# Kernel tuning notes

Hardware: AMD Instinct MI355X
Metric: run time of the kernel (lower is better)

## Reference

```python
import jax, jax.numpy as jnp
import numpy as np

N, D, K = 65536, 512, 512


def _l2norm(x, eps=1e-12):
    # matches torch F.normalize: x / max(||x||, eps)
    n = jnp.linalg.norm(x, axis=-1, keepdims=True)
    return x / jnp.maximum(n, eps)


def setup_inputs() -> dict:
    key = jax.random.key(0)
    k1, k2 = jax.random.split(key)
    return {
        "embeddings": jax.random.normal(k1, (N, D), dtype=jnp.float32),
        "labels": jax.random.randint(k2, (N,), 0, K),
        "w": jnp.asarray(10.0, dtype=jnp.float32),
        "b": jnp.asarray(-5.0, dtype=jnp.float32),
        "num_classes": K,
    }


def reference(embeddings, labels, w, b, num_classes):
    # assumes labels take all values in [0, num_classes) so torch.unique's
    # inverse == labels (holds for the generated inputs: 65536 draws over 512 ids)
    labels = labels.astype(jnp.int32)
    n = embeddings.shape[0]
    emb = _l2norm(embeddings)                                        # [N, D]
    ones = jnp.ones((n,), dtype=emb.dtype)
    counts = jax.ops.segment_sum(ones, labels, num_segments=num_classes)   # [K]
    sums = jax.ops.segment_sum(emb, labels, num_segments=num_classes)      # [K, D]
    centroids = sums / jnp.maximum(counts, 1.0)[:, None]             # [K, D] (NOT re-normalized, per source)
    sims = emb @ centroids.T                                          # [N, K]
    # exclusive centroid for each sample's own class, vectorized over N
    cnt_i = counts[labels]                                            # [N]
    denom = jnp.maximum(cnt_i - 1.0, 1.0)[:, None]
    excl = _l2norm((sums[labels] - emb) / denom)                      # [N, D]
    own = jnp.sum(emb * excl, axis=-1)                                # [N]
    rows = jnp.arange(n)
    cur = sims[rows, labels]
    own = jnp.where(cnt_i > 1.0, own, cur)                            # skip singleton classes
    sims = sims.at[rows, labels].set(own)
    logits = jnp.maximum(w, 1e-6) * sims + b
    logp = jax.nn.log_softmax(logits, axis=-1)
    return -jnp.mean(logp[rows, labels])
```

## Files before the change

### kernel.cpp

```cpp
#include <hip/hip_runtime.h>
#include <hip/hip_bf16.h>

#define N_ROWS 65536
#define DIM    512
#define KCLS   512
#define BUCKET 256
#define CLOG   6.0f

typedef __bf16 bf16x8 __attribute__((ext_vector_type(8)));
typedef float  f32x16 __attribute__((ext_vector_type(16)));

__device__ __forceinline__ float bf2f(ushort u) {
    union { unsigned int i; float f; } v; v.i = ((unsigned int)u) << 16; return v.f;
}

__global__ __launch_bounds__(256) void rnorm_embb_kernel(
    const float* __restrict__ emb, const int* __restrict__ labels,
    ushort* __restrict__ embb, int* __restrict__ counts,
    ushort* __restrict__ order16)
{
    const int tid  = threadIdx.x;
    const int wave = tid >> 6;
    const int lane = tid & 63;
    const int row  = blockIdx.x * 4 + wave;

    const float4* ep = (const float4*)(emb + (size_t)row * DIM + lane * 8);
    const float4 e0 = ep[0], e1 = ep[1];
    float ss = e0.x*e0.x + e0.y*e0.y + e0.z*e0.z + e0.w*e0.w
             + e1.x*e1.x + e1.y*e1.y + e1.z*e1.z + e1.w*e1.w;
    #pragma unroll
    for (int off = 1; off < 64; off <<= 1)
        ss += __shfl_xor(ss, off, 64);
    const float rn = 1.0f / fmaxf(sqrtf(ss), 1e-12f);

    bf16x8 h;
    h[0] = (__bf16)(e0.x * rn); h[1] = (__bf16)(e0.y * rn);
    h[2] = (__bf16)(e0.z * rn); h[3] = (__bf16)(e0.w * rn);
    h[4] = (__bf16)(e1.x * rn); h[5] = (__bf16)(e1.y * rn);
    h[6] = (__bf16)(e1.z * rn); h[7] = (__bf16)(e1.w * rn);
    *(bf16x8*)(embb + (size_t)row * DIM + lane * 8) = h;

    if (lane == 0) {
        const int l   = labels[row];
        const int pos = atomicAdd(&counts[l], 1);
        order16[l * BUCKET + pos] = (ushort)row;
    }
}

__global__ __launch_bounds__(256) void class_sum_kernel(
    const ushort* __restrict__ embb,
    const int* __restrict__ counts, const ushort* __restrict__ order16,
    float* __restrict__ sums, ushort* __restrict__ centb,
    float* __restrict__ S2c)
{
    __shared__ float part[4][DIM];
    __shared__ float s2p[4];

    const int cls  = blockIdx.x;
    const int tid  = threadIdx.x;
    const int wave = tid >> 6;
    const int lane = tid & 63;
    const int cnt  = counts[cls];
    const int base = cls * BUCKET;
    const int d8   = lane * 8;

    float a0v[8] = {}, a1v[8] = {}, a2v[8] = {}, a3v[8] = {};
    int j = wave;
    for (; j + 12 < cnt; j += 16) {
        const int r1 = order16[base + j];
        const int r2 = order16[base + j + 4];
        const int r3 = order16[base + j + 8];
        const int r4 = order16[base + j + 12];
        const uint4 u1 = *(const uint4*)(embb + (size_t)r1 * DIM + d8);
        const uint4 u2 = *(const uint4*)(embb + (size_t)r2 * DIM + d8);
        const uint4 u3 = *(const uint4*)(embb + (size_t)r3 * DIM + d8);
        const uint4 u4 = *(const uint4*)(embb + (size_t)r4 * DIM + d8);
        const ushort* s1 = (const ushort*)&u1;
        const ushort* s2 = (const ushort*)&u2;
        const ushort* s3 = (const ushort*)&u3;
        const ushort* s4 = (const ushort*)&u4;
        #pragma unroll
        for (int q = 0; q < 8; ++q) {
            a0v[q] += bf2f(s1[q]); a1v[q] += bf2f(s2[q]);
            a2v[q] += bf2f(s3[q]); a3v[q] += bf2f(s4[q]);
        }
    }
    for (; j < cnt; j += 4) {
        const int r = order16[base + j];
        const uint4 u = *(const uint4*)(embb + (size_t)r * DIM + d8);
        const ushort* s1 = (const ushort*)&u;
        #pragma unroll
        for (int q = 0; q < 8; ++q) a0v[q] += bf2f(s1[q]);
    }
    #pragma unroll
    for (int q = 0; q < 8; ++q)
        part[wave][d8 + q] = (a0v[q] + a1v[q]) + (a2v[q] + a3v[q]);
    __syncthreads();

    const int d0 = tid * 2;
    const float s0 = part[0][d0]   + part[1][d0]   + part[2][d0]   + part[3][d0];
    const float s1 = part[0][d0+1] + part[1][d0+1] + part[2][d0+1] + part[3][d0+1];
    *(float2*)(sums + (size_t)cls * DIM + d0) = make_float2(s0, s1);
    const float cinv = 1.0f / fmaxf((float)cnt, 1.0f);
    const __bf16 c0 = (__bf16)(s0 * cinv);
    const __bf16 c1 = (__bf16)(s1 * cinv);
    ushort2 cpk;
    cpk.x = *(const ushort*)&c0;
    cpk.y = *(const ushort*)&c1;
    *(ushort2*)(centb + (size_t)cls * DIM + d0) = cpk;

    float p = s0 * s0 + s1 * s1;
    #pragma unroll
    for (int off = 1; off < 64; off <<= 1)
        p += __shfl_xor(p, off, 64);
    if ((tid & 63) == 0) s2p[wave] = p;
    __syncthreads();
    if (tid == 0) S2c[cls] = s2p[0] + s2p[1] + s2p[2] + s2p[3];
}

#define BM   128
#define BN   128
#define BK   64

#define GLDS(g_, l_)                                                          \
    __builtin_amdgcn_global_load_lds(                                         \
        (const __attribute__((address_space(1))) unsigned int*)(g_),          \
        (__attribute__((address_space(3))) unsigned int*)(l_), 16, 0, 0)

#define MFMA(d_, a_, b_) d_ = __builtin_amdgcn_mfma_f32_32x32x16_bf16(a_, b_, d_, 0, 0, 0)

__global__ __launch_bounds__(256, 3) void fused_loss_kernel(
    const ushort* __restrict__ embb, const int* __restrict__ labels,
    const ushort* __restrict__ centb,
    const float* __restrict__ wp, const float* __restrict__ bp,
    float* __restrict__ srow4, float* __restrict__ llgemm)
{
    __shared__ __align__(16) ushort A_lds[8192];
    __shared__ __align__(16) ushort B_lds[8192];
    __shared__ float s_ws[2][BM];
    __shared__ int   lbl_s[BM];

    const int tid  = threadIdx.x;
    const int wid  = tid >> 6;
    const int ln31 = tid & 31;
    const int half = (tid & 63) >> 5;

    const int xcd   = blockIdx.x & 7;
    const int seq   = blockIdx.x >> 3;
    const int panel = seq & 3;
    const int rb    = (seq >> 2) * 8 + xcd;
    const int r0    = rb * BM;
    const int c0    = panel * BN;

    const float wv = fmaxf(wp[0], 1e-6f);
    const float bv = bp[0];

    const ushort* aS[4];
    const ushort* bS[4];
    #pragma unroll
    for (int s = 0; s < 4; ++s) {
        const int G = tid + 256 * s;
        const int R = G >> 4;
        const int q = (G & 15) ^ (R & 15);
        const int r = ((q >> 3) << 6) | R;
        const int j = q & 7;
        aS[s] = embb  + (size_t)(r0 + r) * DIM + j * 8;
        bS[s] = centb + (size_t)(c0 + r) * DIM + j * 8;
    }

    #define STAGE(T_)                                                         \
        { _Pragma("unroll") for (int s = 0; s < 4; ++s) {                     \
            GLDS(aS[s] + (T_) * BK, &A_lds[wid * 512 + s * 2048]);            \
            GLDS(bS[s] + (T_) * BK, &B_lds[wid * 512 + s * 2048]); } }

    const int rg = wid >> 1, cg = wid & 1;
    const int rOff0 = ln31 * 256;
    const int rOff1 = (32 + ln31) * 256;
    const int px    = ln31 & 15;

    f32x16 acc[2][2] = {};

    #pragma unroll 1
    for (int t = 0; t < 8; ++t) {
        STAGE(t);
        __syncthreads();
        const char* aR = (const char*)&A_lds[0];
        const char* bR = (const char*)&B_lds[0];
        #pragma unroll
        for (int ks = 0; ks < 4; ++ks) {
            const int j  = ks * 2 + half;
            const int oA = ((rg * 8 + j) ^ px) << 4;
            const int oB = ((cg * 8 + j) ^ px) << 4;
            const bf16x8 a0 = *(const bf16x8*)(aR + rOff0 + oA);
            const bf16x8 a1 = *(const bf16x8*)(aR + rOff1 + oA);
            const bf16x8 b0 = *(const bf16x8*)(bR + rOff0 + oB);
            const bf16x8 b1 = *(const bf16x8*)(bR + rOff1 + oB);
            MFMA(acc[0][0], a0, b0); MFMA(acc[0][1], a0, b1);
            MFMA(acc[1][0], a1, b0); MFMA(acc[1][1], a1, b1);
        }
        __syncthreads();
    }

    if (tid < BM) lbl_s[tid] = labels[r0 + tid];
    __syncthreads();

    #pragma unroll
    for (int mt = 0; mt < 2; ++mt) {
        #pragma unroll
        for (int reg = 0; reg < 16; ++reg) {
            const int rowc = rg * 64 + mt * 32 + (reg & 3) + 8 * (reg >> 2) + 4 * half;
            const int lloc = lbl_s[rowc] - c0;
            const float v0 = wv * acc[mt][0][reg] + bv;
            const float v1 = wv * acc[mt][1][reg] + bv;
            const int cc = cg * 64 + ln31;
            if (cc == lloc)      llgemm[r0 + rowc] = v0;
            if (cc + 32 == lloc) llgemm[r0 + rowc] = v1;
            float e = __expf(v0 - CLOG) + __expf(v1 - CLOG);
            #pragma unroll
            for (int off = 1; off < 32; off <<= 1)
                e += __shfl_xor(e, off, 64);
            if (ln31 == 0) s_ws[cg][rowc] = e;
        }
    }
    __syncthreads();
    if (tid < BM)
        srow4[(size_t)panel * N_ROWS + r0 + tid] = s_ws[0][tid] + s_ws[1][tid];
}

__global__ __launch_bounds__(256) void merge_loss_kernel(
    const int* __restrict__ labels, const int* __restrict__ counts,
    const float* __restrict__ S2c, const float* __restrict__ srow4,
    const float* __restrict__ llgemm,
    const float* __restrict__ wp, const float* __restrict__ bp,
    float* __restrict__ partial)
{
    __shared__ float red[4];
    const int tid = threadIdx.x;
    const int row = blockIdx.x * 256 + tid;

    const float wv = fmaxf(wp[0], 1e-6f);
    const float bv = bp[0];

    const int lbl = labels[row];
    const int cnt = counts[lbl];
    const float lg = llgemm[row];
    float s = srow4[row] + srow4[N_ROWS + row]
            + srow4[2 * N_ROWS + row] + srow4[3 * N_ROWS + row];
    float ll = lg;
    if (cnt > 1) {
        const float dot = (lg - bv) / wv;
        const float q   = (float)cnt * dot;
        const float nrm = sqrtf(fmaxf(S2c[lbl] - 2.0f * q + 1.0f, 0.0f));
        const float own = (q - 1.0f) / fmaxf(nrm, 1e-12f);
        const float vown = wv * own + bv;
        s += __expf(vown - CLOG) - __expf(lg - CLOG);
        ll = vown;
    }
    float lsum = __logf(s) + CLOG - ll;
    #pragma unroll
    for (int off = 32; off > 0; off >>= 1)
        lsum += __shfl_down(lsum, off, 64);
    if ((tid & 63) == 0) red[tid >> 6] = lsum;
    __syncthreads();
    if (tid == 0)
        partial[blockIdx.x] = red[0] + red[1] + red[2] + red[3];
}

__global__ __launch_bounds__(256) void final_loss_kernel(
    const float* __restrict__ partial, float* __restrict__ out)
{
    __shared__ float red[4];
    const int tid = threadIdx.x;
    float a = partial[tid];
    #pragma unroll
    for (int off = 32; off > 0; off >>= 1)
        a += __shfl_down(a, off, 64);
    if ((tid & 63) == 0) red[tid >> 6] = a;
    __syncthreads();
    if (tid == 0)
        out[0] = (red[0] + red[1] + red[2] + red[3]) / (float)N_ROWS;
}

extern "C" void kernel_launch(void* const* d_in, const int* in_sizes, int n_in,
                              void* d_out, int out_size, void* d_ws, size_t ws_size,
                              hipStream_t stream)
{
    const float* emb    = (const float*)d_in[0];
    const int*   labels = (const int*)d_in[1];
    const float* wp     = (const float*)d_in[2];
    const float* bp     = (const float*)d_in[3];
    float* out = (float*)d_out;

    char* ws = (char*)d_ws;
    ushort* embb    = (ushort*)(ws + 0);
    ushort* order16 = (ushort*)(ws + 67108864);
    float*  sums    = (float*) (ws + 67371008);
    ushort* centb   = (ushort*)(ws + 68419584);
    int*    counts  = (int*)   (ws + 68943872);
    float*  partial = (float*) (ws + 68950016);
    float*  llgemm  = (float*) (ws + 69212160);
    float*  srow4   = (float*) (ws + 69474304);
    float*  S2c     = (float*) (ws + 70522880);

    hipMemsetAsync(counts, 0, 2048, stream);

    rnorm_embb_kernel<<<N_ROWS / 4, 256, 0, stream>>>(emb, labels, embb, counts, order16);
    class_sum_kernel<<<KCLS, 256, 0, stream>>>(embb, counts, order16, sums, centb, S2c);
    fused_loss_kernel<<<2048, 256, 0, stream>>>(embb, labels, centb, wp, bp, srow4, llgemm);
    merge_loss_kernel<<<N_ROWS / 256, 256, 0, stream>>>(labels, counts, S2c, srow4,
                                                        llgemm, wp, bp, partial);
    final_loss_kernel<<<1, 256, 0, stream>>>(partial, out);
}
```

Before: 275.6 us.

## Widen class-sum blocks, drop unused sums, fold final reduction into merge

The class-sum kernel now runs 16 waves per class instead of 4. Each wave takes 4 consecutive rows per step, and the kernel no longer writes the float sums array, which nothing else reads. The separate final-reduction kernel is removed: each merge block bumps an atomic counter, and the last block to finish reduces the per-block partials and writes the loss. This saves one kernel launch and one unused global write, at the cost of a threadfence/atomic per block and an extra zeroed counter in the workspace.

```diff
diff --git a/kernel.cpp b/kernel.cpp
--- a/kernel.cpp
+++ b/kernel.cpp
@@ -47,14 +47,13 @@
     }
 }
 
-__global__ __launch_bounds__(256) void class_sum_kernel(
+__global__ __launch_bounds__(1024) void class_sum_kernel(
     const ushort* __restrict__ embb,
     const int* __restrict__ counts, const ushort* __restrict__ order16,
-    float* __restrict__ sums, ushort* __restrict__ centb,
-    float* __restrict__ S2c)
-{
-    __shared__ float part[4][DIM];
-    __shared__ float s2p[4];
+    ushort* __restrict__ centb, float* __restrict__ S2c)
+{
+    __shared__ float part[16][DIM];
+    __shared__ float s2p[8];
 
     const int cls  = blockIdx.x;
     const int tid  = threadIdx.x;
@@ -65,12 +64,12 @@
     const int d8   = lane * 8;
 
     float a0v[8] = {}, a1v[8] = {}, a2v[8] = {}, a3v[8] = {};
-    int j = wave;
-    for (; j + 12 < cnt; j += 16) {
+    int j = wave * 4;
+    for (; j + 3 < cnt; j += 64) {
         const int r1 = order16[base + j];
-        const int r2 = order16[base + j + 4];
-        const int r3 = order16[base + j + 8];
-        const int r4 = order16[base + j + 12];
+        const int r2 = order16[base + j + 1];
+        const int r3 = order16[base + j + 2];
+        const int r4 = order16[base + j + 3];
         const uint4 u1 = *(const uint4*)(embb + (size_t)r1 * DIM + d8);
         const uint4 u2 = *(const uint4*)(embb + (size_t)r2 * DIM + d8);
         const uint4 u3 = *(const uint4*)(embb + (size_t)r3 * DIM + d8);
@@ -85,8 +84,8 @@
             a2v[q] += bf2f(s3[q]); a3v[q] += bf2f(s4[q]);
         }
     }
-    for (; j < cnt; j += 4) {
-        const int r = order16[base + j];
+    for (int t2 = j; t2 < cnt; ++t2) {
+        const int r = order16[base + t2];
         const uint4 u = *(const uint4*)(embb + (size_t)r * DIM + d8);
         const ushort* s1 = (const ushort*)&u;
         #pragma unroll
@@ -97,25 +96,26 @@
         part[wave][d8 + q] = (a0v[q] + a1v[q]) + (a2v[q] + a3v[q]);
     __syncthreads();
 
-    const int d0 = tid * 2;
-    const float s0 = part[0][d0]   + part[1][d0]   + part[2][d0]   + part[3][d0];
-    const float s1 = part[0][d0+1] + part[1][d0+1] + part[2][d0+1] + part[3][d0+1];
-    *(float2*)(sums + (size_t)cls * DIM + d0) = make_float2(s0, s1);
-    const float cinv = 1.0f / fmaxf((float)cnt, 1.0f);
-    const __bf16 c0 = (__bf16)(s0 * cinv);
-    const __bf16 c1 = (__bf16)(s1 * cinv);
-    ushort2 cpk;
-    cpk.x = *(const ushort*)&c0;
-    cpk.y = *(const ushort*)&c1;
-    *(ushort2*)(centb + (size_t)cls * DIM + d0) = cpk;
-
-    float p = s0 * s0 + s1 * s1;
-    #pragma unroll
-    for (int off = 1; off < 64; off <<= 1)
-        p += __shfl_xor(p, off, 64);
-    if ((tid & 63) == 0) s2p[wave] = p;
-    __syncthreads();
-    if (tid == 0) S2c[cls] = s2p[0] + s2p[1] + s2p[2] + s2p[3];
+    if (tid < DIM) {
+        float s = 0.f;
+        #pragma unroll
+        for (int w = 0; w < 16; ++w) s += part[w][tid];
+        const float cinv = 1.0f / fmaxf((float)cnt, 1.0f);
+        const __bf16 c = (__bf16)(s * cinv);
+        centb[(size_t)cls * DIM + tid] = *(const ushort*)&c;
+        float p = s * s;
+        #pragma unroll
+        for (int off = 1; off < 64; off <<= 1)
+            p += __shfl_xor(p, off, 64);
+        if (lane == 0) s2p[wave] = p;
+    }
+    __syncthreads();
+    if (tid == 0) {
+        float t = 0.f;
+        #pragma unroll
+        for (int w = 0; w < 8; ++w) t += s2p[w];
+        S2c[cls] = t;
+    }
 }
 
 #define BM   128
@@ -232,9 +232,11 @@
     const float* __restrict__ S2c, const float* __restrict__ srow4,
     const float* __restrict__ llgemm,
     const float* __restrict__ wp, const float* __restrict__ bp,
-    float* __restrict__ partial)
+    float* __restrict__ partial, int* __restrict__ done,
+    float* __restrict__ out)
 {
     __shared__ float red[4];
+    __shared__ int   last_s;
     const int tid = threadIdx.x;
     const int row = blockIdx.x * 256 + tid;
 
@@ -262,23 +264,23 @@
         lsum += __shfl_down(lsum, off, 64);
     if ((tid & 63) == 0) red[tid >> 6] = lsum;
     __syncthreads();
-    if (tid == 0)
+    if (tid == 0) {
         partial[blockIdx.x] = red[0] + red[1] + red[2] + red[3];
-}
-
-__global__ __launch_bounds__(256) void final_loss_kernel(
-    const float* __restrict__ partial, float* __restrict__ out)
-{
-    __shared__ float red[4];
-    const int tid = threadIdx.x;
-    float a = partial[tid];
-    #pragma unroll
-    for (int off = 32; off > 0; off >>= 1)
-        a += __shfl_down(a, off, 64);
-    if ((tid & 63) == 0) red[tid >> 6] = a;
-    __syncthreads();
-    if (tid == 0)
-        out[0] = (red[0] + red[1] + red[2] + red[3]) / (float)N_ROWS;
+        __threadfence();
+        last_s = (atomicAdd(done, 1) == (N_ROWS / 256) - 1) ? 1 : 0;
+    }
+    __syncthreads();
+    if (last_s) {
+        float a = __hip_atomic_load(&partial[tid], __ATOMIC_RELAXED,
+                                    __HIP_MEMORY_SCOPE_AGENT);
+        #pragma unroll
+        for (int off = 32; off > 0; off >>= 1)
+            a += __shfl_down(a, off, 64);
+        if ((tid & 63) == 0) red[tid >> 6] = a;
+        __syncthreads();
+        if (tid == 0)
+            out[0] = (red[0] + red[1] + red[2] + red[3]) / (float)N_ROWS;
+    }
 }
 
 extern "C" void kernel_launch(void* const* d_in, const int* in_sizes, int n_in,
@@ -294,20 +296,20 @@
     char* ws = (char*)d_ws;
     ushort* embb    = (ushort*)(ws + 0);
     ushort* order16 = (ushort*)(ws + 67108864);
-    float*  sums    = (float*) (ws + 67371008);
     ushort* centb   = (ushort*)(ws + 68419584);
     int*    counts  = (int*)   (ws + 68943872);
+    int*    done    = (int*)   (ws + 68945924);
     float*  partial = (float*) (ws + 68950016);
     float*  llgemm  = (float*) (ws + 69212160);
     float*  srow4   = (float*) (ws + 69474304);
     float*  S2c     = (float*) (ws + 70522880);
 
-    hipMemsetAsync(counts, 0, 2048, stream);
+    hipMemsetAsync(counts, 0, 2056, stream);
 
     rnorm_embb_kernel<<<N_ROWS / 4, 256, 0, stream>>>(emb, labels, embb, counts, order16);
-    class_sum_kernel<<<KCLS, 256, 0, stream>>>(embb, counts, order16, sums, centb, S2c);
+    class_sum_kernel<<<KCLS, 1024, 0, stream>>>(embb, counts, order16, centb, S2c);
     fused_loss_kernel<<<2048, 256, 0, stream>>>(embb, labels, centb, wp, bp, srow4, llgemm);
     merge_loss_kernel<<<N_ROWS / 256, 256, 0, stream>>>(labels, counts, S2c, srow4,
-                                                        llgemm, wp, bp, partial);
-    final_loss_kernel<<<1, 256, 0, stream>>>(partial, out);
-}
+                                                        llgemm, wp, bp,
+                                                        partial, done, out);
+}
```

Measured after the change: 282.0 us. 2.3% more time.

## Enlarge GEMM tiles with triple-buffered async LDS pipeline and fuse final reduction

Applied to the files above, without the earlier changes.

Moves the fused similarity/logsumexp GEMM to 256x256 tiles with 512 threads and BK=32. It adds a three-stage global_load_lds ring buffer with explicit vmcnt waits, so loads overlap MFMA work and each panel loads less A data. The final reduction kernel is folded into merge_loss through a last-block atomic counter, and the unused sums write is dropped. The risks are larger LDS use, which lowers occupancy, and hand-managed waitcnt correctness.

```diff
diff --git a/kernel.cpp b/kernel.cpp
--- a/kernel.cpp
+++ b/kernel.cpp
@@ -50,8 +50,7 @@
 __global__ __launch_bounds__(256) void class_sum_kernel(
     const ushort* __restrict__ embb,
     const int* __restrict__ counts, const ushort* __restrict__ order16,
-    float* __restrict__ sums, ushort* __restrict__ centb,
-    float* __restrict__ S2c)
+    ushort* __restrict__ centb, float* __restrict__ S2c)
 {
     __shared__ float part[4][DIM];
     __shared__ float s2p[4];
@@ -100,7 +99,6 @@
     const int d0 = tid * 2;
     const float s0 = part[0][d0]   + part[1][d0]   + part[2][d0]   + part[3][d0];
     const float s1 = part[0][d0+1] + part[1][d0+1] + part[2][d0+1] + part[3][d0+1];
-    *(float2*)(sums + (size_t)cls * DIM + d0) = make_float2(s0, s1);
     const float cinv = 1.0f / fmaxf((float)cnt, 1.0f);
     const __bf16 c0 = (__bf16)(s0 * cinv);
     const __bf16 c1 = (__bf16)(s1 * cinv);
@@ -118,9 +116,9 @@
     if (tid == 0) S2c[cls] = s2p[0] + s2p[1] + s2p[2] + s2p[3];
 }
 
-#define BM   128
-#define BN   128
-#define BK   64
+#define BM   256
+#define BN   256
+#define BK   32
 
 #define GLDS(g_, l_)                                                          \
     __builtin_amdgcn_global_load_lds(                                         \
@@ -129,112 +127,131 @@
 
 #define MFMA(d_, a_, b_) d_ = __builtin_amdgcn_mfma_f32_32x32x16_bf16(a_, b_, d_, 0, 0, 0)
 
-__global__ __launch_bounds__(256, 3) void fused_loss_kernel(
+__global__ __launch_bounds__(512, 2) void fused_loss_kernel(
     const ushort* __restrict__ embb, const int* __restrict__ labels,
     const ushort* __restrict__ centb,
     const float* __restrict__ wp, const float* __restrict__ bp,
-    float* __restrict__ srow4, float* __restrict__ llgemm)
-{
-    __shared__ __align__(16) ushort A_lds[8192];
-    __shared__ __align__(16) ushort B_lds[8192];
-    __shared__ float s_ws[2][BM];
+    float* __restrict__ srow2, float* __restrict__ llgemm)
+{
+    __shared__ __align__(16) ushort A_lds[3 * 8192];
+    __shared__ __align__(16) ushort B_lds[3 * 8192];
+    __shared__ float s_ws[4][BM];
     __shared__ int   lbl_s[BM];
 
     const int tid  = threadIdx.x;
     const int wid  = tid >> 6;
     const int ln31 = tid & 31;
     const int half = (tid & 63) >> 5;
+    const int wm   = wid >> 2;
+    const int wn   = wid & 3;
 
     const int xcd   = blockIdx.x & 7;
     const int seq   = blockIdx.x >> 3;
-    const int panel = seq & 3;
-    const int rb    = (seq >> 2) * 8 + xcd;
+    const int panel = seq & 1;
+    const int rb    = (seq >> 1) * 8 + xcd;
     const int r0    = rb * BM;
     const int c0    = panel * BN;
 
     const float wv = fmaxf(wp[0], 1e-6f);
     const float bv = bp[0];
 
-    const ushort* aS[4];
-    const ushort* bS[4];
-    #pragma unroll
-    for (int s = 0; s < 4; ++s) {
-        const int G = tid + 256 * s;
+    const ushort* aS[2];
+    const ushort* bS[2];
+    #pragma unroll
+    for (int s = 0; s < 2; ++s) {
+        const int G = tid + 512 * s;
         const int R = G >> 4;
         const int q = (G & 15) ^ (R & 15);
-        const int r = ((q >> 3) << 6) | R;
-        const int j = q & 7;
+        const int r = (q >> 2) * 64 + R;
+        const int j = q & 3;
         aS[s] = embb  + (size_t)(r0 + r) * DIM + j * 8;
         bS[s] = centb + (size_t)(c0 + r) * DIM + j * 8;
     }
 
-    #define STAGE(T_)                                                         \
-        { _Pragma("unroll") for (int s = 0; s < 4; ++s) {                     \
-            GLDS(aS[s] + (T_) * BK, &A_lds[wid * 512 + s * 2048]);            \
-            GLDS(bS[s] + (T_) * BK, &B_lds[wid * 512 + s * 2048]); } }
-
-    const int rg = wid >> 1, cg = wid & 1;
-    const int rOff0 = ln31 * 256;
-    const int rOff1 = (32 + ln31) * 256;
-    const int px    = ln31 & 15;
-
-    f32x16 acc[2][2] = {};
-
+    #define STAGE(T_, b_)                                                     \
+        { _Pragma("unroll") for (int s = 0; s < 2; ++s) {                     \
+            GLDS(aS[s] + (T_) * BK, &A_lds[(b_) * 8192 + (tid + 512 * s) * 8]); \
+            GLDS(bS[s] + (T_) * BK, &B_lds[(b_) * 8192 + (tid + 512 * s) * 8]); } }
+
+    f32x16 acc[4][2] = {};
+
+    STAGE(0, 0);
+    STAGE(1, 1);
+    STAGE(2, 2);
+
+    const int pxk = ln31 & 15;
+    const int gA0 = wm * 2, gA1 = wm * 2 + 1;
+
+    int bsel = 0;
     #pragma unroll 1
-    for (int t = 0; t < 8; ++t) {
-        STAGE(t);
-        __syncthreads();
-        const char* aR = (const char*)&A_lds[0];
-        const char* bR = (const char*)&B_lds[0];
-        #pragma unroll
-        for (int ks = 0; ks < 4; ++ks) {
-            const int j  = ks * 2 + half;
-            const int oA = ((rg * 8 + j) ^ px) << 4;
-            const int oB = ((cg * 8 + j) ^ px) << 4;
-            const bf16x8 a0 = *(const bf16x8*)(aR + rOff0 + oA);
-            const bf16x8 a1 = *(const bf16x8*)(aR + rOff1 + oA);
-            const bf16x8 b0 = *(const bf16x8*)(bR + rOff0 + oB);
-            const bf16x8 b1 = *(const bf16x8*)(bR + rOff1 + oB);
+    for (int t = 0; t < 16; ++t) {
+        if (t < 14)       asm volatile("s_waitcnt vmcnt(8)" ::: "memory");
+        else if (t == 14) asm volatile("s_waitcnt vmcnt(4)" ::: "memory");
+        else              asm volatile("s_waitcnt vmcnt(0)" ::: "memory");
+        __builtin_amdgcn_s_barrier();
+        __builtin_amdgcn_sched_barrier(0);
+        const char* aR = (const char*)(A_lds + bsel * 8192);
+        const char* bR = (const char*)(B_lds + bsel * 8192);
+        #pragma unroll
+        for (int ks = 0; ks < 2; ++ks) {
+            const int j = ks * 2 + half;
+            const int oA0 = ((gA0 * 4 + j) ^ pxk) << 4;
+            const int oA1 = ((gA1 * 4 + j) ^ pxk) << 4;
+            const int oB  = ((wn  * 4 + j) ^ pxk) << 4;
+            const bf16x8 a0 = *(const bf16x8*)(aR + ln31 * 256        + oA0);
+            const bf16x8 a1 = *(const bf16x8*)(aR + (32 + ln31) * 256 + oA0);
+            const bf16x8 a2 = *(const bf16x8*)(aR + ln31 * 256        + oA1);
+            const bf16x8 a3 = *(const bf16x8*)(aR + (32 + ln31) * 256 + oA1);
+            const bf16x8 b0 = *(const bf16x8*)(bR + ln31 * 256        + oB);
+            const bf16x8 b1 = *(const bf16x8*)(bR + (32 + ln31) * 256 + oB);
             MFMA(acc[0][0], a0, b0); MFMA(acc[0][1], a0, b1);
             MFMA(acc[1][0], a1, b0); MFMA(acc[1][1], a1, b1);
+            MFMA(acc[2][0], a2, b0); MFMA(acc[2][1], a2, b1);
+            MFMA(acc[3][0], a3, b0); MFMA(acc[3][1], a3, b1);
         }
-        __syncthreads();
+        __builtin_amdgcn_sched_barrier(0);
+        __builtin_amdgcn_s_barrier();
+        if (t + 3 < 16) STAGE(t + 3, bsel);
+        bsel = (bsel == 2) ? 0 : bsel + 1;
     }
 
     if (tid < BM) lbl_s[tid] = labels[r0 + tid];
     __syncthreads();
 
     #pragma unroll
-    for (int mt = 0; mt < 2; ++mt) {
+    for (int rg = 0; rg < 4; ++rg) {
         #pragma unroll
         for (int reg = 0; reg < 16; ++reg) {
-            const int rowc = rg * 64 + mt * 32 + (reg & 3) + 8 * (reg >> 2) + 4 * half;
+            const int rowc = wm * 128 + rg * 32 + (reg & 3) + 8 * (reg >> 2) + 4 * half;
             const int lloc = lbl_s[rowc] - c0;
-            const float v0 = wv * acc[mt][0][reg] + bv;
-            const float v1 = wv * acc[mt][1][reg] + bv;
-            const int cc = cg * 64 + ln31;
+            const float v0 = wv * acc[rg][0][reg] + bv;
+            const float v1 = wv * acc[rg][1][reg] + bv;
+            const int cc = wn * 64 + ln31;
             if (cc == lloc)      llgemm[r0 + rowc] = v0;
             if (cc + 32 == lloc) llgemm[r0 + rowc] = v1;
             float e = __expf(v0 - CLOG) + __expf(v1 - CLOG);
             #pragma unroll
             for (int off = 1; off < 32; off <<= 1)
                 e += __shfl_xor(e, off, 64);
-            if (ln31 == 0) s_ws[cg][rowc] = e;
+            if (ln31 == 0) s_ws[wn][rowc] = e;
         }
     }
     __syncthreads();
     if (tid < BM)
-        srow4[(size_t)panel * N_ROWS + r0 + tid] = s_ws[0][tid] + s_ws[1][tid];
+        srow2[(size_t)panel * N_ROWS + r0 + tid] =
+            (s_ws[0][tid] + s_ws[1][tid]) + (s_ws[2][tid] + s_ws[3][tid]);
 }
 
 __global__ __launch_bounds__(256) void merge_loss_kernel(
     const int* __restrict__ labels, const int* __restrict__ counts,
-    const float* __restrict__ S2c, const float* __restrict__ srow4,
+    const float* __restrict__ S2c, const float* __restrict__ srow2,
     const float* __restrict__ llgemm,
     const float* __restrict__ wp, const float* __restrict__ bp,
-    float* __restrict__ partial)
+    float* __restrict__ partial, int* __restrict__ done,
+    float* __restrict__ out)
 {
     __shared__ float red[4];
+    __shared__ int   last_s;
     const int tid = threadIdx.x;
     const int row = blockIdx.x * 256 + tid;
 
@@ -244,8 +261,7 @@
     const int lbl = labels[row];
     const int cnt = counts[lbl];
     const float lg = llgemm[row];
-    float s = srow4[row] + srow4[N_ROWS + row]
-            + srow4[2 * N_ROWS + row] + srow4[3 * N_ROWS + row];
+    float s = srow2[row] + srow2[N_ROWS + row];
     float ll = lg;
     if (cnt > 1) {
         const float dot = (lg - bv) / wv;
@@ -262,23 +278,23 @@
         lsum += __shfl_down(lsum, off, 64);
     if ((tid & 63) == 0) red[tid >> 6] = lsum;
     __syncthreads();
-    if (tid == 0)
+    if (tid == 0) {
         partial[blockIdx.x] = red[0] + red[1] + red[2] + red[3];
-}
-
-__global__ __launch_bounds__(256) void final_loss_kernel(
-    const float* __restrict__ partial, float* __restrict__ out)
-{
-    __shared__ float red[4];
-    const int tid = threadIdx.x;
-    float a = partial[tid];
-    #pragma unroll
-    for (int off = 32; off > 0; off >>= 1)
-        a += __shfl_down(a, off, 64);
-    if ((tid & 63) == 0) red[tid >> 6] = a;
-    __syncthreads();
-    if (tid == 0)
-        out[0] = (red[0] + red[1] + red[2] + red[3]) / (float)N_ROWS;
+        __threadfence();
+        last_s = (atomicAdd(done, 1) == (N_ROWS / 256) - 1) ? 1 : 0;
+    }
+    __syncthreads();
+    if (last_s) {
+        float a = __hip_atomic_load(&partial[tid], __ATOMIC_RELAXED,
+                                    __HIP_MEMORY_SCOPE_AGENT);
+        #pragma unroll
+        for (int off = 32; off > 0; off >>= 1)
+            a += __shfl_down(a, off, 64);
+        if ((tid & 63) == 0) red[tid >> 6] = a;
+        __syncthreads();
+        if (tid == 0)
+            out[0] = (red[0] + red[1] + red[2] + red[3]) / (float)N_ROWS;
+    }
 }
 
 extern "C" void kernel_launch(void* const* d_in, const int* in_sizes, int n_in,
@@ -294,20 +310,20 @@
     char* ws = (char*)d_ws;
     ushort* embb    = (ushort*)(ws + 0);
     ushort* order16 = (ushort*)(ws + 67108864);
-    float*  sums    = (float*) (ws + 67371008);
     ushort* centb   = (ushort*)(ws + 68419584);
     int*    counts  = (int*)   (ws + 68943872);
+    int*    done    = (int*)   (ws + 68945924);
     float*  partial = (float*) (ws + 68950016);
     float*  llgemm  = (float*) (ws + 69212160);
-    float*  srow4   = (float*) (ws + 69474304);
+    float*  srow2   = (float*) (ws + 69474304);
     float*  S2c     = (float*) (ws + 70522880);
 
-    hipMemsetAsync(counts, 0, 2048, stream);
+    hipMemsetAsync(counts, 0, 2056, stream);
 
     rnorm_embb_kernel<<<N_ROWS / 4, 256, 0, stream>>>(emb, labels, embb, counts, order16);
-    class_sum_kernel<<<KCLS, 256, 0, stream>>>(embb, counts, order16, sums, centb, S2c);
-    fused_loss_kernel<<<2048, 256, 0, stream>>>(embb, labels, centb, wp, bp, srow4, llgemm);
-    merge_loss_kernel<<<N_ROWS / 256, 256, 0, stream>>>(labels, counts, S2c, srow4,
-                                                        llgemm, wp, bp, partial);
-    final_loss_kernel<<<1, 256, 0, stream>>>(partial, out);
-}
+    class_sum_kernel<<<KCLS, 256, 0, stream>>>(embb, counts, order16, centb, S2c);
+    fused_loss_kernel<<<512, 512, 0, stream>>>(embb, labels, centb, wp, bp, srow2, llgemm);
+    merge_loss_kernel<<<N_ROWS / 256, 256, 0, stream>>>(labels, counts, S2c, srow2,
+                                                        llgemm, wp, bp,
+                                                        partial, done, out);
+}
```

Result: slower. 302.4 us (+9.7%).
